# Kernel tuning notes

Hardware: AMD Instinct MI355X
Metric: run time of the kernel (lower is better)

The kernel has to match this reference:

```python
import jax, jax.numpy as jnp
import numpy as np

# Grid / problem constants (match init_kwargs: shape=[15,400,400], batch_size=2)
B, D, H, W = 2, 15, 400, 400
N = 200000          # active voxels
CIN, COUT = 32, 64
# 27 kernel offsets for ksize=3, dilation=1, centered (submanifold alignment)
OFFS = np.array([[dz, dy, dx]
                 for dz in (-1, 0, 1)
                 for dy in (-1, 0, 1)
                 for dx in (-1, 0, 1)], dtype=np.int32)  # [27, 3]


def setup_inputs() -> dict:
    rng = np.random.default_rng(0)
    # unique active voxel coordinates (sorted flat indices for locality)
    flat = np.sort(rng.choice(B * D * H * W, size=N, replace=False)).astype(np.int64)
    b = flat // (D * H * W)
    r = flat % (D * H * W)
    z = r // (H * W)
    r = r % (H * W)
    y = r // W
    x = r % W
    coors = jnp.asarray(np.stack([b, z, y, x], axis=1).astype(np.int32))  # [N,4]

    key = jax.random.key(0)
    k1, k2, k3 = jax.random.split(key, 3)
    features = jax.random.normal(k1, (N, CIN), jnp.float32)
    W1 = jax.random.normal(k2, (27, CIN, COUT), jnp.float32) * (1.0 / np.sqrt(27.0 * CIN))
    W2 = jax.random.normal(k3, (27, COUT, COUT), jnp.float32) * (1.0 / np.sqrt(27.0 * COUT))
    return {"features": features, "coors": coors, "batch_size": B, "W1": W1, "W2": W2}


def _neighbor_table(coors):
    """Rulebook: for each of 27 offsets, index of the neighboring active voxel (-1 if none)."""
    n = coors.shape[0]
    flat = ((coors[:, 0] * D + coors[:, 1]) * H + coors[:, 2]) * W + coors[:, 3]
    # dense voxel hash: flat coord -> row index, -1 = inactive
    table = jnp.full((B * D * H * W,), -1, jnp.int32).at[flat].set(
        jnp.arange(n, dtype=jnp.int32))
    offs = jnp.asarray(OFFS)  # [27,3]
    z = coors[None, :, 1] + offs[:, 0:1]  # [27,N]
    y = coors[None, :, 2] + offs[:, 1:2]
    x = coors[None, :, 3] + offs[:, 2:3]
    valid = (z >= 0) & (z < D) & (y >= 0) & (y < H) & (x >= 0) & (x < W)
    nflat = ((coors[None, :, 0] * D + jnp.clip(z, 0, D - 1)) * H
             + jnp.clip(y, 0, H - 1)) * W + jnp.clip(x, 0, W - 1)
    nbr = table[nflat]                      # [27, N]
    return jnp.where(valid, nbr, -1)


def _subm_conv(feats, nbr, Wk):
    """Gather-GEMM-scatter submanifold conv: out[i] = sum_k W[k] @ feats[nbr[k,i]]."""
    out = jnp.zeros((feats.shape[0], Wk.shape[-1]), feats.dtype)
    for k in range(nbr.shape[0]):  # fixed 27-iteration loop over kernel offsets
        j = nbr[k]
        valid = j >= 0
        g = jnp.where(valid[:, None], feats[jnp.where(valid, j, 0)], 0.0)  # [N,Cin]
        out = out + g @ Wk[k]
    return out


def reference(features, coors, batch_size, W1, W2):
    # Submanifold conv preserves the active set -> rulebook is shared by both layers.
    nbr = _neighbor_table(coors)
    x = _subm_conv(features, nbr, W1)   # [N, COUT]
    x = _subm_conv(x, nbr, W2)          # [N, COUT]
    return x
```

## Files before the change

kernel.cpp:

```cpp
#include <hip/hip_runtime.h>
#include <hip/hip_bf16.h>

#define DD 15
#define HH 400
#define WW 400
#define CIN 32
#define COUT 64
#define KK 27
#define NVOX (2 * DD * HH * WW)
#define NWORDS (NVOX / 64)
#define CAP 32768
#define CNT_STRIDE 64
#define OFFC_GRID 1024
#define PCAP 262144
#define SCAN_B 1024

typedef short bf16x8 __attribute__((ext_vector_type(8)));
typedef float f32x4  __attribute__((ext_vector_type(4)));

__device__ inline short f2bf(float f) {
    unsigned u = __float_as_uint(f);
    return (short)((u + 0x7FFFu + ((u >> 16) & 1u)) >> 16);
}
__device__ inline float bflo(unsigned u) { return __uint_as_float(u << 16); }
__device__ inline float bfhi(unsigned u) { return __uint_as_float(u & 0xFFFF0000u); }

__global__ void init_kernel(unsigned long long* __restrict__ bitmap,
                            int* __restrict__ cnt) {
    int t = blockIdx.x * blockDim.x + threadIdx.x;
    if (t < KK * CNT_STRIDE) cnt[t] = 0;
    int stride = gridDim.x * blockDim.x;
    for (int w = t; w < NWORDS; w += stride) bitmap[w] = 0ull;
}

__global__ void fill_kernel(const int* __restrict__ coors,
                            int* __restrict__ flats,
                            unsigned long long* __restrict__ bitmap, int n) {
    int i = blockIdx.x * blockDim.x + threadIdx.x;
    if (i >= n) return;
    int b = coors[i * 4 + 0];
    int z = coors[i * 4 + 1];
    int y = coors[i * 4 + 2];
    int x = coors[i * 4 + 3];
    int f = ((b * DD + z) * HH + y) * WW + x;
    flats[i] = f;
    atomicOr(&bitmap[f >> 6], 1ull << (f & 63));
}

__global__ void prefix_kernel(const int* __restrict__ flats,
                              int* __restrict__ prefix, int n) {
    int w = blockIdx.x * blockDim.x + threadIdx.x;
    if (w >= NWORDS) return;
    int target = w << 6;
    int lo = 0, hi = n;
    while (lo < hi) {
        int mid = (lo + hi) >> 1;
        if (flats[mid] < target) lo = mid + 1; else hi = mid;
    }
    prefix[w] = lo;
}

__device__ inline bool bm_test(const unsigned long long* __restrict__ bitmap, int f) {
    return (bitmap[f >> 6] >> (f & 63)) & 1ull;
}
__device__ inline int bm_rank(const unsigned long long* __restrict__ bitmap,
                              const int* __restrict__ prefix, int f) {
    int w = f >> 6, b = f & 63;
    unsigned long long m = bitmap[w];
    return prefix[w] + __popcll(m & ((1ull << b) - 1ull));
}

__global__ __launch_bounds__(256) void build_pairs_kernel(
        const int* __restrict__ flats,
        const unsigned long long* __restrict__ bitmap,
        const int* __restrict__ prefix,
        int* __restrict__ cnt, int* __restrict__ pairI,
        int* __restrict__ pairJ, int* __restrict__ percnt, int n) {
    __shared__ int lcnt[KK];
    __shared__ int lbase[KK];
    __shared__ int lpos[KK];
    int i = blockIdx.x * blockDim.x + threadIdx.x;
    if (threadIdx.x < KK) { lcnt[threadIdx.x] = 0; lpos[threadIdx.x] = 0; }
    __syncthreads();

    int f0 = 0, x = 0;
    unsigned vmask = 0;
    bool act = (i < n);
    if (act) {
        f0 = flats[i];
        x = f0 % WW;
        int rem = f0 / WW;
        int y = rem % HH;
        int z = (rem / HH) % DD;
#pragma unroll
        for (int p = 0; p < 9; ++p) {
            int dz = p / 3 - 1, dy = p % 3 - 1;
            int zn = z + dz, yn = y + dy;
            if (zn < 0 || zn >= DD || yn < 0 || yn >= HH) continue;
            int fn = f0 + dz * (HH * WW) + dy * WW;
            int kb = p * 3;
            if (x > 0 && bm_test(bitmap, fn - 1)) {
                vmask |= 1u << kb; atomicAdd(&lcnt[kb], 1);
            }
            if (kb + 1 != 13 && bm_test(bitmap, fn)) {
                vmask |= 1u << (kb + 1); atomicAdd(&lcnt[kb + 1], 1);
            }
            if (x < WW - 1 && bm_test(bitmap, fn + 1)) {
                vmask |= 1u << (kb + 2); atomicAdd(&lcnt[kb + 2], 1);
            }
        }
        percnt[i] = __popc(vmask);
    }
    __syncthreads();
    if (threadIdx.x < KK && lcnt[threadIdx.x] > 0)
        lbase[threadIdx.x] = atomicAdd(&cnt[threadIdx.x * CNT_STRIDE], lcnt[threadIdx.x]);
    __syncthreads();
    if (act && vmask) {
        int lt = 0;
#pragma unroll
        for (int p = 0; p < 9; ++p) {
            int kb = p * 3;
            if (!(vmask & (7u << kb))) continue;
            int dz = p / 3 - 1, dy = p % 3 - 1;
            int fn = f0 + dz * (HH * WW) + dy * WW;
#pragma unroll
            for (int d = 0; d < 3; ++d) {
                int k = kb + d;
                if (!(vmask & (1u << k))) continue;
                int j = bm_rank(bitmap, prefix, fn + d - 1);
                int pos = lbase[k] + atomicAdd(&lpos[k], 1);
                if (pos < CAP) {
                    pairI[k * CAP + pos] = (i << 5) | lt;
                    pairJ[k * CAP + pos] = j;
                }
                ++lt;
            }
        }
    }
}

__global__ void scan1pad_kernel(const int* __restrict__ pc, int* __restrict__ bsum,
                                const int* __restrict__ cnt, int* __restrict__ pairI,
                                int* __restrict__ pairJ, int n, int nscan) {
    __shared__ int red[256];
    if ((int)blockIdx.x >= nscan) {
        int k = blockIdx.x - nscan;
        int ck = min(cnt[k * CNT_STRIDE], CAP);
        int ckp = min((ck + 127) & ~127, CAP);
        for (int pos = ck + (int)threadIdx.x; pos < ckp; pos += blockDim.x) {
            pairI[k * CAP + pos] = (n << 5);
            pairJ[k * CAP + pos] = 0;
        }
        return;
    }
    int base = blockIdx.x * SCAN_B;
    int s = 0;
#pragma unroll
    for (int u = 0; u < 4; ++u) {
        int idx = base + u * 256 + threadIdx.x;
        if (idx < n) s += pc[idx];
    }
    red[threadIdx.x] = s; __syncthreads();
    for (int o = 128; o > 0; o >>= 1) {
        if ((int)threadIdx.x < o) red[threadIdx.x] += red[threadIdx.x + o];
        __syncthreads();
    }
    if (threadIdx.x == 0) bsum[blockIdx.x] = red[0];
}

__global__ void scan3_kernel(const int* __restrict__ pc, const int* __restrict__ bsum,
                             int* __restrict__ rowptr, int n, int nscan) {
    __shared__ int ts[256];
    __shared__ int bs[256];
    int v = ((int)threadIdx.x < nscan && (int)threadIdx.x < (int)blockIdx.x)
                ? bsum[threadIdx.x] : 0;
    bs[threadIdx.x] = v; __syncthreads();
    for (int o = 128; o > 0; o >>= 1) {
        if ((int)threadIdx.x < o) bs[threadIdx.x] += bs[threadIdx.x + o];
        __syncthreads();
    }
    int bbase = bs[0];

    int base = blockIdx.x * SCAN_B + threadIdx.x * 4;
    int e[4]; int s = 0;
#pragma unroll
    for (int u = 0; u < 4; ++u) {
        int idx = base + u;
        e[u] = (idx < n) ? pc[idx] : 0;
        s += e[u];
    }
    ts[threadIdx.x] = s; __syncthreads();
    for (int o = 1; o < 256; o <<= 1) {
        int t = ((int)threadIdx.x >= o) ? ts[threadIdx.x - o] : 0;
        __syncthreads();
        ts[threadIdx.x] += t;
        __syncthreads();
    }
    int run = ts[threadIdx.x] - s + bbase;
#pragma unroll
    for (int u = 0; u < 4; ++u) {
        int idx = base + u;
        if (idx < n) rowptr[idx] = run;
        run += e[u];
        if (idx == n - 1) rowptr[n] = run;
    }
}

template <int C, typename TIN, typename TOUT>
__global__ __launch_bounds__(256) void center_mfma_kernel(
        const TIN* __restrict__ xin, const float* __restrict__ Wc,
        const int* __restrict__ rowptr, const unsigned short* __restrict__ part,
        TOUT* __restrict__ xout, int n) {
    constexpr int KT = C / 32;
    int lane = threadIdx.x & 63;
    int mrow = lane & 15;
    int kgrp = lane >> 4;
    int wid = (blockIdx.x * blockDim.x + threadIdx.x) >> 6;
    int nwaves = (gridDim.x * blockDim.x) >> 6;

    bf16x8 bf[KT][4];
#pragma unroll
    for (int kt = 0; kt < KT; ++kt)
#pragma unroll
        for (int nt = 0; nt < 4; ++nt)
#pragma unroll
            for (int j = 0; j < 8; ++j)
                bf[kt][nt][j] = f2bf(Wc[(kt * 32 + kgrp * 8 + j) * 64 + nt * 16 + mrow]);

    int ntiles = (n + 15) >> 4;
    for (int t = wid; t < ntiles; t += nwaves) {
        int row = t * 16 + mrow;
        f32x4 zero = {0.f, 0.f, 0.f, 0.f};
        bf16x8 a[KT];
        if (row < n) {
            if constexpr (sizeof(TIN) == 4) {
                const float* xr = (const float*)xin + (size_t)row * C + kgrp * 8;
#pragma unroll
                for (int kt = 0; kt < KT; ++kt) {
                    float4 x0 = *(const float4*)(xr + kt * 32);
                    float4 x1 = *(const float4*)(xr + kt * 32 + 4);
                    a[kt][0] = f2bf(x0.x); a[kt][1] = f2bf(x0.y);
                    a[kt][2] = f2bf(x0.z); a[kt][3] = f2bf(x0.w);
                    a[kt][4] = f2bf(x1.x); a[kt][5] = f2bf(x1.y);
                    a[kt][6] = f2bf(x1.z); a[kt][7] = f2bf(x1.w);
                }
            } else {
                const unsigned short* xr = (const unsigned short*)xin + (size_t)row * C + kgrp * 8;
#pragma unroll
                for (int kt = 0; kt < KT; ++kt)
                    a[kt] = *(const bf16x8*)(xr + kt * 32);
            }
        } else {
#pragma unroll
            for (int kt = 0; kt < KT; ++kt)
#pragma unroll
                for (int j = 0; j < 8; ++j) a[kt][j] = 0;
        }
        f32x4 acc[4];
#pragma unroll
        for (int nt = 0; nt < 4; ++nt) {
            acc[nt] = zero;
#pragma unroll
            for (int kt = 0; kt < KT; ++kt)
                acc[nt] = __builtin_amdgcn_mfma_f32_16x16x32_bf16(a[kt], bf[kt][nt], acc[nt], 0, 0, 0);
        }
#pragma unroll
        for (int r = 0; r < 4; ++r) {
            int orow = t * 16 + kgrp * 4 + r;
            if (orow < n) {
                int s0 = rowptr[orow], s1 = rowptr[orow + 1];
                for (int s = s0; s < s1; ++s) {
                    uint2 q = *(const uint2*)(part + (size_t)s * 64 + mrow * 4);
                    acc[0][r] += bflo(q.x);
                    acc[1][r] += bfhi(q.x);
                    acc[2][r] += bflo(q.y);
                    acc[3][r] += bfhi(q.y);
                }
                if constexpr (sizeof(TOUT) == 4) {
#pragma unroll
                    for (int nt = 0; nt < 4; ++nt)
                        ((float*)xout)[(size_t)orow * 64 + nt * 16 + mrow] = acc[nt][r];
                } else {
#pragma unroll
                    for (int nt = 0; nt < 4; ++nt)
                        ((unsigned short*)xout)[(size_t)orow * 64 + nt * 16 + mrow] =
                            (unsigned short)f2bf(acc[nt][r]);
                }
            }
        }
    }
}

template <int C, typename TIN>
__global__ __launch_bounds__(256) void offc_mfma_kernel(
        const TIN* __restrict__ xin, const float* __restrict__ Wsrc,
        const int* __restrict__ cnt, const int* __restrict__ pairI,
        const int* __restrict__ pairJ, const int* __restrict__ rowptr,
        unsigned short* __restrict__ part, int n) {
    constexpr int KT = C / 32;
    __shared__ int pfx[KK + 1];
    int lane = threadIdx.x & 63;
    int wid = threadIdx.x >> 6;
    int mrow = lane & 15;
    int kgrp = lane >> 4;
    if (threadIdx.x == 0) {
        int acc = 0; pfx[0] = 0;
        for (int k = 0; k < KK; ++k) {
            int ck = min(cnt[k * CNT_STRIDE], CAP);
            acc += (ck + 127) >> 7;
            pfx[k + 1] = acc;
        }
    }
    __syncthreads();
    int T = pfx[KK];
    int span = (T + gridDim.x - 1) / gridDim.x;
    int g0 = blockIdx.x * span;
    int g1 = min(g0 + span, T);
    int kcur = -1;
    bf16x8 bf[KT][4];
    for (int g = g0; g < g1; ++g) {
        int k = (kcur < 0) ? 0 : kcur;
        while (pfx[k + 1] <= g) ++k;
        if (k != kcur) {
            const float* Wk = Wsrc + (size_t)k * C * 64;
#pragma unroll
            for (int kt = 0; kt < KT; ++kt)
#pragma unroll
                for (int nt = 0; nt < 4; ++nt)
#pragma unroll
                    for (int j = 0; j < 8; ++j)
                        bf[kt][nt][j] = f2bf(Wk[(kt * 32 + kgrp * 8 + j) * 64 + nt * 16 + mrow]);
            kcur = k;
        }
        int chunk = g - pfx[k];
        int base = k * CAP + chunk * 128 + wid * 32;
#pragma unroll
        for (int half = 0; half < 2; ++half) {
            int b16 = base + half * 16;
            int jrow = pairJ[b16 + mrow];
            bf16x8 a[KT];
            if constexpr (sizeof(TIN) == 4) {
                const float* xr = (const float*)xin + (size_t)jrow * C + kgrp * 8;
#pragma unroll
                for (int kt = 0; kt < KT; ++kt) {
                    float4 x0 = *(const float4*)(xr + kt * 32);
                    float4 x1 = *(const float4*)(xr + kt * 32 + 4);
                    a[kt][0] = f2bf(x0.x); a[kt][1] = f2bf(x0.y);
                    a[kt][2] = f2bf(x0.z); a[kt][3] = f2bf(x0.w);
                    a[kt][4] = f2bf(x1.x); a[kt][5] = f2bf(x1.y);
                    a[kt][6] = f2bf(x1.z); a[kt][7] = f2bf(x1.w);
                }
            } else {
                const unsigned short* xr = (const unsigned short*)xin + (size_t)jrow * C + kgrp * 8;
#pragma unroll
                for (int kt = 0; kt < KT; ++kt)
                    a[kt] = *(const bf16x8*)(xr + kt * 32);
            }
            f32x4 zero = {0.f, 0.f, 0.f, 0.f};
            f32x4 acc[4];
#pragma unroll
            for (int nt = 0; nt < 4; ++nt) {
                acc[nt] = zero;
#pragma unroll
                for (int kt = 0; kt < KT; ++kt)
                    acc[nt] = __builtin_amdgcn_mfma_f32_16x16x32_bf16(a[kt], bf[kt][nt], acc[nt], 0, 0, 0);
            }
#pragma unroll
            for (int r = 0; r < 4; ++r) {
                int pk = pairI[b16 + kgrp * 4 + r];
                int ir = pk >> 5;
                if (ir < n) {
                    int dst = rowptr[ir] + (pk & 31);
                    if (dst < PCAP) {
                        uint2 q;
                        q.x = (unsigned)(unsigned short)f2bf(acc[0][r]) |
                              ((unsigned)(unsigned short)f2bf(acc[1][r]) << 16);
                        q.y = (unsigned)(unsigned short)f2bf(acc[2][r]) |
                              ((unsigned)(unsigned short)f2bf(acc[3][r]) << 16);
                        *(uint2*)(part + (size_t)dst * 64 + mrow * 4) = q;
                    }
                }
            }
        }
    }
}

extern "C" void kernel_launch(void* const* d_in, const int* in_sizes, int n_in,
                              void* d_out, int out_size, void* d_ws, size_t ws_size,
                              hipStream_t stream) {
    const float* feats = (const float*)d_in[0];
    const int*   coors = (const int*)d_in[1];
    const float* W1 = (const float*)d_in[3];
    const float* W2 = (const float*)d_in[4];
    float* out = (float*)d_out;

    int n = in_sizes[0] / CIN;

    char* ws = (char*)d_ws;
    size_t off = 0;
    unsigned short* x1 = (unsigned short*)(ws + off);
    off += ((size_t)n * COUT * 2 + 255) & ~(size_t)255;
    unsigned long long* bitmap = (unsigned long long*)(ws + off);
    off += ((size_t)NWORDS * 8 + 255) & ~(size_t)255;
    int* prefix = (int*)(ws + off);
    off += ((size_t)NWORDS * 4 + 255) & ~(size_t)255;
    int* flats = (int*)(ws + off);
    off += ((size_t)n * 4 + 255) & ~(size_t)255;
    int* percnt = (int*)(ws + off);
    off += ((size_t)n * 4 + 255) & ~(size_t)255;
    int* rowptr = (int*)(ws + off);
    off += ((size_t)(n + 1) * 4 + 255) & ~(size_t)255;
    int* bsum = (int*)(ws + off);
    off += (256 * 4 + 255) & ~(size_t)255;
    int* cnt = (int*)(ws + off);
    off += ((size_t)KK * CNT_STRIDE * 4 + 255) & ~(size_t)255;
    int* pairI = (int*)(ws + off);
    off += ((size_t)KK * CAP * 4 + 4096 + 255) & ~(size_t)255;
    int* pairJ = (int*)(ws + off);
    off += ((size_t)KK * CAP * 4 + 4096 + 255) & ~(size_t)255;
    unsigned short* part = (unsigned short*)(ws + off);

    int nscan = (n + SCAN_B - 1) / SCAN_B;
    int ntiles = (n + 15) / 16;
    int cgrid = (ntiles + 3) / 4;

    init_kernel<<<(NWORDS + 255) / 256, 256, 0, stream>>>(bitmap, cnt);
    fill_kernel<<<(n + 255) / 256, 256, 0, stream>>>(coors, flats, bitmap, n);
    prefix_kernel<<<(NWORDS + 255) / 256, 256, 0, stream>>>(flats, prefix, n);
    build_pairs_kernel<<<(n + 255) / 256, 256, 0, stream>>>(
        flats, bitmap, prefix, cnt, pairI, pairJ, percnt, n);
    scan1pad_kernel<<<nscan + KK, 256, 0, stream>>>(percnt, bsum, cnt, pairI, pairJ, n, nscan);
    scan3_kernel<<<nscan, 256, 0, stream>>>(percnt, bsum, rowptr, n, nscan);
    offc_mfma_kernel<CIN, float><<<OFFC_GRID, 256, 0, stream>>>(
        feats, W1, cnt, pairI, pairJ, rowptr, part, n);
    center_mfma_kernel<CIN, float, unsigned short><<<cgrid, 256, 0, stream>>>(
        feats, W1 + (size_t)13 * CIN * COUT, rowptr, part, x1, n);
    offc_mfma_kernel<COUT, unsigned short><<<OFFC_GRID, 256, 0, stream>>>(
        x1, W2, cnt, pairI, pairJ, rowptr, part, n);
    center_mfma_kernel<COUT, unsigned short, float><<<cgrid, 256, 0, stream>>>(
        x1, W2 + (size_t)13 * COUT * COUT, rowptr, part, out, n);
}
```

Measured before the change: 149.9 us.

## Fuse rulebook prelude kernels into one kernel using software grid barriers

Replaces the separate init, fill, prefix, build_pairs, scan1pad and scan3 launches with one prelude kernel. Its phases are separated by atomic-counter grid barriers, and zeroing moves to two hipMemsetAsync calls. Block sums are now produced per 256-thread block during pair building, and the row-pointer scan and padding run in later phases of the same kernel. The aim is to remove kernel-launch gaps and inter-kernel drains. In exchange, the code assumes all 782 blocks are co-resident, which a normal launch does not guarantee, so the barriers could deadlock; it also adds spin-wait cost at each barrier.

```diff
diff --git a/kernel.cpp b/kernel.cpp
--- a/kernel.cpp
+++ b/kernel.cpp
@@ -25,41 +25,6 @@
 __device__ inline float bflo(unsigned u) { return __uint_as_float(u << 16); }
 __device__ inline float bfhi(unsigned u) { return __uint_as_float(u & 0xFFFF0000u); }
 
-__global__ void init_kernel(unsigned long long* __restrict__ bitmap,
-                            int* __restrict__ cnt) {
-    int t = blockIdx.x * blockDim.x + threadIdx.x;
-    if (t < KK * CNT_STRIDE) cnt[t] = 0;
-    int stride = gridDim.x * blockDim.x;
-    for (int w = t; w < NWORDS; w += stride) bitmap[w] = 0ull;
-}
-
-__global__ void fill_kernel(const int* __restrict__ coors,
-                            int* __restrict__ flats,
-                            unsigned long long* __restrict__ bitmap, int n) {
-    int i = blockIdx.x * blockDim.x + threadIdx.x;
-    if (i >= n) return;
-    int b = coors[i * 4 + 0];
-    int z = coors[i * 4 + 1];
-    int y = coors[i * 4 + 2];
-    int x = coors[i * 4 + 3];
-    int f = ((b * DD + z) * HH + y) * WW + x;
-    flats[i] = f;
-    atomicOr(&bitmap[f >> 6], 1ull << (f & 63));
-}
-
-__global__ void prefix_kernel(const int* __restrict__ flats,
-                              int* __restrict__ prefix, int n) {
-    int w = blockIdx.x * blockDim.x + threadIdx.x;
-    if (w >= NWORDS) return;
-    int target = w << 6;
-    int lo = 0, hi = n;
-    while (lo < hi) {
-        int mid = (lo + hi) >> 1;
-        if (flats[mid] < target) lo = mid + 1; else hi = mid;
-    }
-    prefix[w] = lo;
-}
-
 __device__ inline bool bm_test(const unsigned long long* __restrict__ bitmap, int f) {
     return (bitmap[f >> 6] >> (f & 63)) & 1ull;
 }
@@ -70,24 +35,59 @@
     return prefix[w] + __popcll(m & ((1ull << b) - 1ull));
 }
 
-__global__ __launch_bounds__(256) void build_pairs_kernel(
-        const int* __restrict__ flats,
-        const unsigned long long* __restrict__ bitmap,
-        const int* __restrict__ prefix,
-        int* __restrict__ cnt, int* __restrict__ pairI,
-        int* __restrict__ pairJ, int* __restrict__ percnt, int n) {
+__device__ inline void grid_barrier(int* ctr, int nblk) {
+    __syncthreads();
+    if (threadIdx.x == 0) {
+        __threadfence();
+        atomicAdd(ctr, 1);
+        while (atomicAdd(ctr, 0) < nblk) { __builtin_amdgcn_s_sleep(8); }
+    }
+    __syncthreads();
+}
+
+__global__ __launch_bounds__(256) void prelude_kernel(
+        const int* __restrict__ coors, int* __restrict__ flats,
+        unsigned long long* __restrict__ bitmap, int* __restrict__ prefix,
+        int* __restrict__ cnt, int* __restrict__ pairI, int* __restrict__ pairJ,
+        int* __restrict__ percnt, int* __restrict__ bsum, int* __restrict__ rowptr,
+        int* __restrict__ ctr, int n, int nscan) {
     __shared__ int lcnt[KK];
     __shared__ int lbase[KK];
     __shared__ int lpos[KK];
+    __shared__ int sh[256];
+    __shared__ int sh2[256];
     int i = blockIdx.x * blockDim.x + threadIdx.x;
+    int nblk = gridDim.x;
+    bool act = (i < n);
+
+    int f0 = 0;
+    if (act) {
+        int b = coors[i * 4 + 0];
+        int z = coors[i * 4 + 1];
+        int y = coors[i * 4 + 2];
+        int x = coors[i * 4 + 3];
+        f0 = ((b * DD + z) * HH + y) * WW + x;
+        flats[i] = f0;
+        atomicOr(&bitmap[f0 >> 6], 1ull << (f0 & 63));
+    }
+    grid_barrier(&ctr[0], nblk);
+
+    if (i < NWORDS) {
+        int target = i << 6;
+        int lo = 0, hi = n;
+        while (lo < hi) {
+            int mid = (lo + hi) >> 1;
+            if (flats[mid] < target) lo = mid + 1; else hi = mid;
+        }
+        prefix[i] = lo;
+    }
+    grid_barrier(&ctr[1], nblk);
+
     if (threadIdx.x < KK) { lcnt[threadIdx.x] = 0; lpos[threadIdx.x] = 0; }
     __syncthreads();
-
-    int f0 = 0, x = 0;
     unsigned vmask = 0;
-    bool act = (i < n);
+    int x = 0;
     if (act) {
-        f0 = flats[i];
         x = f0 % WW;
         int rem = f0 / WW;
         int y = rem % HH;
@@ -111,9 +111,15 @@
         }
         percnt[i] = __popc(vmask);
     }
+    sh[threadIdx.x] = act ? (int)__popc(vmask) : 0;
     __syncthreads();
     if (threadIdx.x < KK && lcnt[threadIdx.x] > 0)
         lbase[threadIdx.x] = atomicAdd(&cnt[threadIdx.x * CNT_STRIDE], lcnt[threadIdx.x]);
+    for (int o = 128; o > 0; o >>= 1) {
+        if ((int)threadIdx.x < o) sh[threadIdx.x] += sh[threadIdx.x + o];
+        __syncthreads();
+    }
+    if (threadIdx.x == 0) atomicExch(&bsum[blockIdx.x], sh[0]);
     __syncthreads();
     if (act && vmask) {
         int lt = 0;
@@ -137,72 +143,50 @@
             }
         }
     }
-}
-
-__global__ void scan1pad_kernel(const int* __restrict__ pc, int* __restrict__ bsum,
-                                const int* __restrict__ cnt, int* __restrict__ pairI,
-                                int* __restrict__ pairJ, int n, int nscan) {
-    __shared__ int red[256];
-    if ((int)blockIdx.x >= nscan) {
-        int k = blockIdx.x - nscan;
-        int ck = min(cnt[k * CNT_STRIDE], CAP);
+    grid_barrier(&ctr[2], nblk);
+
+    int bid = blockIdx.x;
+    if (bid < nscan) {
+        int lim = 4 * bid;
+        int v = 0;
+        for (int j = threadIdx.x; j < lim; j += 256) v += atomicAdd(&bsum[j], 0);
+        sh2[threadIdx.x] = v; __syncthreads();
+        for (int o = 128; o > 0; o >>= 1) {
+            if ((int)threadIdx.x < o) sh2[threadIdx.x] += sh2[threadIdx.x + o];
+            __syncthreads();
+        }
+        int bbase = sh2[0];
+        int base = bid * SCAN_B + threadIdx.x * 4;
+        int e[4]; int s = 0;
+#pragma unroll
+        for (int u = 0; u < 4; ++u) {
+            int idx = base + u;
+            e[u] = (idx < n) ? percnt[idx] : 0;
+            s += e[u];
+        }
+        sh[threadIdx.x] = s; __syncthreads();
+        for (int o = 1; o < 256; o <<= 1) {
+            int t = ((int)threadIdx.x >= o) ? sh[threadIdx.x - o] : 0;
+            __syncthreads();
+            sh[threadIdx.x] += t;
+            __syncthreads();
+        }
+        int run = sh[threadIdx.x] - s + bbase;
+#pragma unroll
+        for (int u = 0; u < 4; ++u) {
+            int idx = base + u;
+            if (idx < n) rowptr[idx] = run;
+            run += e[u];
+            if (idx == n - 1) rowptr[n] = run;
+        }
+    } else if (bid < nscan + KK) {
+        int k = bid - nscan;
+        int ck = min(atomicAdd(&cnt[k * CNT_STRIDE], 0), CAP);
         int ckp = min((ck + 127) & ~127, CAP);
-        for (int pos = ck + (int)threadIdx.x; pos < ckp; pos += blockDim.x) {
+        for (int pos = ck + (int)threadIdx.x; pos < ckp; pos += 256) {
             pairI[k * CAP + pos] = (n << 5);
             pairJ[k * CAP + pos] = 0;
         }
-        return;
-    }
-    int base = blockIdx.x * SCAN_B;
-    int s = 0;
-#pragma unroll
-    for (int u = 0; u < 4; ++u) {
-        int idx = base + u * 256 + threadIdx.x;
-        if (idx < n) s += pc[idx];
-    }
-    red[threadIdx.x] = s; __syncthreads();
-    for (int o = 128; o > 0; o >>= 1) {
-        if ((int)threadIdx.x < o) red[threadIdx.x] += red[threadIdx.x + o];
-        __syncthreads();
-    }
-    if (threadIdx.x == 0) bsum[blockIdx.x] = red[0];
-}
-
-__global__ void scan3_kernel(const int* __restrict__ pc, const int* __restrict__ bsum,
-                             int* __restrict__ rowptr, int n, int nscan) {
-    __shared__ int ts[256];
-    __shared__ int bs[256];
-    int v = ((int)threadIdx.x < nscan && (int)threadIdx.x < (int)blockIdx.x)
-                ? bsum[threadIdx.x] : 0;
-    bs[threadIdx.x] = v; __syncthreads();
-    for (int o = 128; o > 0; o >>= 1) {
-        if ((int)threadIdx.x < o) bs[threadIdx.x] += bs[threadIdx.x + o];
-        __syncthreads();
-    }
-    int bbase = bs[0];
-
-    int base = blockIdx.x * SCAN_B + threadIdx.x * 4;
-    int e[4]; int s = 0;
-#pragma unroll
-    for (int u = 0; u < 4; ++u) {
-        int idx = base + u;
-        e[u] = (idx < n) ? pc[idx] : 0;
-        s += e[u];
-    }
-    ts[threadIdx.x] = s; __syncthreads();
-    for (int o = 1; o < 256; o <<= 1) {
-        int t = ((int)threadIdx.x >= o) ? ts[threadIdx.x - o] : 0;
-        __syncthreads();
-        ts[threadIdx.x] += t;
-        __syncthreads();
-    }
-    int run = ts[threadIdx.x] - s + bbase;
-#pragma unroll
-    for (int u = 0; u < 4; ++u) {
-        int idx = base + u;
-        if (idx < n) rowptr[idx] = run;
-        run += e[u];
-        if (idx == n - 1) rowptr[n] = run;
     }
 }
 
@@ -411,26 +395,27 @@
     int* rowptr = (int*)(ws + off);
     off += ((size_t)(n + 1) * 4 + 255) & ~(size_t)255;
     int* bsum = (int*)(ws + off);
-    off += (256 * 4 + 255) & ~(size_t)255;
+    off += (1024 * 4 + 255) & ~(size_t)255;
     int* cnt = (int*)(ws + off);
-    off += ((size_t)KK * CNT_STRIDE * 4 + 255) & ~(size_t)255;
+    size_t cntbytes = (size_t)(KK * CNT_STRIDE + 64) * 4;
+    int* ctr = cnt + KK * CNT_STRIDE;
+    off += (cntbytes + 255) & ~(size_t)255;
     int* pairI = (int*)(ws + off);
     off += ((size_t)KK * CAP * 4 + 4096 + 255) & ~(size_t)255;
     int* pairJ = (int*)(ws + off);
     off += ((size_t)KK * CAP * 4 + 4096 + 255) & ~(size_t)255;
     unsigned short* part = (unsigned short*)(ws + off);
 
+    int nbuild = (n + 255) / 256;
     int nscan = (n + SCAN_B - 1) / SCAN_B;
     int ntiles = (n + 15) / 16;
     int cgrid = (ntiles + 3) / 4;
 
-    init_kernel<<<(NWORDS + 255) / 256, 256, 0, stream>>>(bitmap, cnt);
-    fill_kernel<<<(n + 255) / 256, 256, 0, stream>>>(coors, flats, bitmap, n);
-    prefix_kernel<<<(NWORDS + 255) / 256, 256, 0, stream>>>(flats, prefix, n);
-    build_pairs_kernel<<<(n + 255) / 256, 256, 0, stream>>>(
-        flats, bitmap, prefix, cnt, pairI, pairJ, percnt, n);
-    scan1pad_kernel<<<nscan + KK, 256, 0, stream>>>(percnt, bsum, cnt, pairI, pairJ, n, nscan);
-    scan3_kernel<<<nscan, 256, 0, stream>>>(percnt, bsum, rowptr, n, nscan);
+    hipMemsetAsync(bitmap, 0, (size_t)NWORDS * 8, stream);
+    hipMemsetAsync(cnt, 0, cntbytes, stream);
+    prelude_kernel<<<nbuild, 256, 0, stream>>>(
+        coors, flats, bitmap, prefix, cnt, pairI, pairJ, percnt, bsum, rowptr,
+        ctr, n, nscan);
     offc_mfma_kernel<CIN, float><<<OFFC_GRID, 256, 0, stream>>>(
         feats, W1, cnt, pairI, pairJ, rowptr, part, n);
     center_mfma_kernel<CIN, float, unsigned short><<<cgrid, 256, 0, stream>>>(
```

After: 353.8 us. 2.36x slower.
